# Optimization experiments

Measured on AMD Instinct MI355X. Metric: run time of the kernel, lower is better.

The kernel has to match this reference:

```python
import jax, jax.numpy as jnp
import numpy as np

B = 100000      # query points
L = 8           # num levels
N_RBF = 256     # RBF centers per level
F = 16          # features per level
OUT = 3         # output dim


def setup_inputs() -> dict:
    key = jax.random.key(0)
    k = jax.random.split(key, 6)
    x = jax.random.normal(k[0], (B, 3), dtype=jnp.float32)
    # small-magnitude features so gaussian RBF responses are non-degenerate
    feats = 0.1 * jax.random.normal(k[1], (B, L * F), dtype=jnp.float32)
    # centers initialized uniform(-1e-4, 1e-4) as in the torch module
    centers = jax.random.uniform(k[2], (L, N_RBF, F), dtype=jnp.float32,
                                 minval=-1e-4, maxval=1e-4)
    # log-width parameters (exp'd in forward); small perturbation around 0
    betas = 0.01 * jax.random.normal(k[3], (L, N_RBF, F), dtype=jnp.float32)
    W = jax.random.normal(k[4], (OUT, N_RBF * L), dtype=jnp.float32) / np.sqrt(N_RBF * L)
    b = jax.random.normal(k[5], (OUT,), dtype=jnp.float32) * 0.01
    return {"x": x, "feats": feats, "centers": centers, "betas": betas, "W": W, "b": b}


def reference(x, feats, centers, betas, W, b):
    # centers, betas: [L, N, F]. x is unused by the original forward (faithful).
    Lnum, N, f = centers.shape
    rbfs = []
    for i in range(Lnum):
        # concat of first i+1 per-level tables along feature axis -> [N, (i+1)*f]
        C = centers[: i + 1].transpose(1, 0, 2).reshape(N, (i + 1) * f)
        Bw = jnp.exp(betas[: i + 1].transpose(1, 0, 2).reshape(N, (i + 1) * f))
        x_in = feats[:, : (i + 1) * f]                      # [B, (i+1)*f]
        term1 = (x_in * x_in) @ Bw.T                        # [B, N]
        term2 = x_in @ (Bw * C).T                           # [B, N]
        term3 = jnp.sum(Bw * C * C, axis=1)                 # [N]
        dist_sq = term1 - 2.0 * term2 + term3[None, :]
        rbfs.append(jnp.exp(-0.5 * dist_sq))                # gaussian basis
    outs = jnp.concatenate(rbfs, axis=-1)                   # [B, L*N]
    return outs @ W.T + b
```

## Files before the change

### kernel.cpp

```cpp
#include <hip/hip_runtime.h>
#include <math.h>

#define LN 8
#define NRBF 256
#define FD 16
#define OUTD 3
#define KC (-0.72134752044f)

typedef __attribute__((ext_vector_type(8))) short short8;
typedef __attribute__((ext_vector_type(4))) float floatx4;
typedef __attribute__((ext_vector_type(2))) float floatx2;

__device__ __forceinline__ short f2bf(float f) {
    unsigned u = __builtin_bit_cast(unsigned, f);
    u += 0x7fffu + ((u >> 16) & 1u);
    return (short)(u >> 16);
}


__global__ __launch_bounds__(256) void prep(
    const float* __restrict__ centers, const float* __restrict__ betas,
    const float* __restrict__ W, short* __restrict__ PKB, float* __restrict__ EPI)
{
    __shared__ float ls[LN * 32];
    int blk = blockIdx.x;
    int tid = threadIdx.x;
    if (blk < 32) {
        int t = blk * 256 + tid;
        int lane = t & 63;
        int nt   = (t >> 6) & 15;
        int j    = t >> 10;
        int n    = nt * 16 + (lane & 15);
        int kq   = lane >> 4;
        size_t base = ((size_t)(j * NRBF + n)) * FD + kq * 4;
        float4 bq = *(const float4*)(betas + base);
        float4 cq = *(const float4*)(centers + base);
        float a0 = __expf(bq.x), a1 = __expf(bq.y), a2 = __expf(bq.z), a3 = __expf(bq.w);
        short8 v;
        v[0] = f2bf(a0); v[1] = f2bf(-2.0f * a0 * cq.x);
        v[2] = f2bf(a1); v[3] = f2bf(-2.0f * a1 * cq.y);
        v[4] = f2bf(a2); v[5] = f2bf(-2.0f * a2 * cq.z);
        v[6] = f2bf(a3); v[7] = f2bf(-2.0f * a3 * cq.w);
        *((short8*)(PKB + (size_t)((nt * 8 + j) * 64 + lane) * 8)) = v;
    } else {
        int jj = tid >> 5;
        int nl = tid & 31;
        int n  = (blk - 32) * 32 + nl;
        const float* bp = betas   + ((size_t)(jj * NRBF + n)) * FD;
        const float* cp = centers + ((size_t)(jj * NRBF + n)) * FD;
        float s = 0.f;
#pragma unroll
        for (int q = 0; q < 4; ++q) {
            float4 bq = *(const float4*)(bp + q * 4);
            float4 cq = *(const float4*)(cp + q * 4);
            s = fmaf(__expf(bq.x) * cq.x, cq.x, s);
            s = fmaf(__expf(bq.y) * cq.y, cq.y, s);
            s = fmaf(__expf(bq.z) * cq.z, cq.z, s);
            s = fmaf(__expf(bq.w) * cq.w, cq.w, s);
        }
        ls[jj * 32 + nl] = s;
        __syncthreads();
        float t3 = 0.f;
        for (int j2 = 0; j2 <= jj; ++j2) t3 += ls[j2 * 32 + nl];
        float4 e;
        e.x = KC * t3;
        e.y = W[0 * (LN * NRBF) + jj * NRBF + n];
        e.z = W[1 * (LN * NRBF) + jj * NRBF + n];
        e.w = W[2 * (LN * NRBF) + jj * NRBF + n];
        int nt = n >> 4, l = n & 15;
        ((float4*)EPI)[nt * 128 + jj * 16 + l] = e;
    }
}

__global__ __launch_bounds__(256, 4) void rbf_mfma(
    const float* __restrict__ feats, const short* __restrict__ PKB,
    const float* __restrict__ EPI, const float* __restrict__ bias,
    float* __restrict__ out, int B)
{
    int tid  = threadIdx.x;
    int lane = tid & 63;
    int wid  = tid >> 6;
    int ntile_total = (B + 15) >> 4;
    int tile = blockIdx.x * 4 + wid;
    bool tvalid = (tile < ntile_total);
    if (!tvalid) tile = ntile_total - 1;
    int b0 = tile * 16;
    int m  = lane & 15;
    int kq = lane >> 4;

    int brow = b0 + m; if (brow >= B) brow = B - 1;
    const float* xrow = feats + (size_t)brow * (LN * FD) + kq * 4;
    short8 afrag[LN];
#pragma unroll
    for (int j = 0; j < LN; ++j) {
        float4 x = *((const float4*)(xrow + j * FD));
        short8 f;
        f[0] = f2bf(x.x * x.x); f[1] = f2bf(x.x);
        f[2] = f2bf(x.y * x.y); f[3] = f2bf(x.y);
        f[4] = f2bf(x.z * x.z); f[5] = f2bf(x.z);
        f[6] = f2bf(x.w * x.w); f[7] = f2bf(x.w);
        afrag[j] = f;
    }

    floatx2 o01[4];
    float   o2[4];
#pragma unroll
    for (int r = 0; r < 4; ++r) { o01[r] = (floatx2){0.f, 0.f}; o2[r] = 0.f; }

#pragma unroll 1
    for (int nt = 0; nt < 8; ++nt) {
        const short8* pb0 = (const short8*)PKB + (size_t)(nt * 8) * 64 + lane;
        const short8* pb1 = pb0 + (size_t)8 * 8 * 64;
        const float4* ep0 = (const float4*)EPI + (size_t)nt * 128 + m;
        const float4* ep1 = ep0 + (size_t)8 * 128;
        floatx4 acc0 = {0.f, 0.f, 0.f, 0.f};
        floatx4 acc1 = {0.f, 0.f, 0.f, 0.f};
#pragma unroll
        for (int j = 0; j < LN; ++j) {
            short8 bf0 = pb0[j * 64];
            short8 bf1 = pb1[j * 64];
            float4 e0  = ep0[j * 16];
            float4 e1  = ep1[j * 16];
            acc0 = __builtin_amdgcn_mfma_f32_16x16x32_bf16(afrag[j], bf0, acc0, 0, 0, 0);
            acc1 = __builtin_amdgcn_mfma_f32_16x16x32_bf16(afrag[j], bf1, acc1, 0, 0, 0);
            floatx2 eyz0 = {e0.y, e0.z};
            floatx2 eyz1 = {e1.y, e1.z};
#pragma unroll
            for (int r = 0; r < 4; ++r) {
                float rv0 = __builtin_amdgcn_exp2f(fmaf(acc0[r], KC, e0.x));
                float rv1 = __builtin_amdgcn_exp2f(fmaf(acc1[r], KC, e1.x));
                floatx2 rv02 = {rv0, rv0};
                floatx2 rv12 = {rv1, rv1};
                o01[r] += rv02 * eyz0;
                o01[r] += rv12 * eyz1;
                o2[r]   = fmaf(rv0, e0.w, o2[r]);
                o2[r]   = fmaf(rv1, e1.w, o2[r]);
            }
        }
    }

    float oacc[12];
#pragma unroll
    for (int r = 0; r < 4; ++r) {
        oacc[r * 3 + 0] = o01[r].x;
        oacc[r * 3 + 1] = o01[r].y;
        oacc[r * 3 + 2] = o2[r];
    }
#pragma unroll
    for (int i = 0; i < 12; ++i) {
        oacc[i] += __shfl_xor(oacc[i], 1);
        oacc[i] += __shfl_xor(oacc[i], 2);
        oacc[i] += __shfl_xor(oacc[i], 4);
        oacc[i] += __shfl_xor(oacc[i], 8);
    }

    if (tvalid && m < OUTD) {
        float bv = bias[m];
#pragma unroll
        for (int r = 0; r < 4; ++r) {
            int row = b0 + kq * 4 + r;
            if (row < B) out[(size_t)row * OUTD + m] = oacc[r * 3 + m] + bv;
        }
    }
}

extern "C" void kernel_launch(void* const* d_in, const int* in_sizes, int n_in,
                              void* d_out, int out_size, void* d_ws, size_t ws_size,
                              hipStream_t stream) {
    const float* feats   = (const float*)d_in[1];
    const float* centers = (const float*)d_in[2];
    const float* betas   = (const float*)d_in[3];
    const float* W       = (const float*)d_in[4];
    const float* bias    = (const float*)d_in[5];
    float* out = (float*)d_out;
    int B = in_sizes[1] / (LN * FD);

    short* PKB = (short*)d_ws;
    float* EPI = (float*)((char*)d_ws + 65536 * 2);

    prep<<<40, 256, 0, stream>>>(centers, betas, W, PKB, EPI);

    int tiles  = (B + 15) / 16;
    int blocks = (tiles + 3) / 4;
    rbf_mfma<<<blocks, 256, 0, stream>>>(feats, PKB, EPI, bias, out, B);
}
```

Baseline: 161.1 us.

## Stage packed RBF weights in LDS via double-buffered async loads, loop levels outer

Reorders the main loop so the level index is outermost and all 16 N-tiles keep their accumulators live in registers. For each level, the packed B fragments and epilogue constants are staged into shared memory with double-buffered global_load_lds, so the four waves of a block share one copy instead of each wave loading from global/L2. The prep kernel's output layout is changed to match level-major staging. This adds 64 accumulator VGPRs and a barrier per level, and lowers the occupancy hint from 4 to 3 waves per SIMD.

```diff
diff --git a/kernel.cpp b/kernel.cpp
--- a/kernel.cpp
+++ b/kernel.cpp
@@ -41,7 +41,7 @@
         v[2] = f2bf(a1); v[3] = f2bf(-2.0f * a1 * cq.y);
         v[4] = f2bf(a2); v[5] = f2bf(-2.0f * a2 * cq.z);
         v[6] = f2bf(a3); v[7] = f2bf(-2.0f * a3 * cq.w);
-        *((short8*)(PKB + (size_t)((nt * 8 + j) * 64 + lane) * 8)) = v;
+        *((short8*)(PKB + (size_t)t * 8)) = v;
     } else {
         int jj = tid >> 5;
         int nl = tid & 31;
@@ -68,20 +68,23 @@
         e.z = W[1 * (LN * NRBF) + jj * NRBF + n];
         e.w = W[2 * (LN * NRBF) + jj * NRBF + n];
         int nt = n >> 4, l = n & 15;
-        ((float4*)EPI)[nt * 128 + jj * 16 + l] = e;
-    }
-}
-
-__global__ __launch_bounds__(256, 4) void rbf_mfma(
+        ((float4*)EPI)[(jj * 16 + nt) * 16 + l] = e;
+    }
+}
+
+__global__ __launch_bounds__(256, 3) void rbf_mfma(
     const float* __restrict__ feats, const short* __restrict__ PKB,
     const float* __restrict__ EPI, const float* __restrict__ bias,
     float* __restrict__ out, int B)
 {
+    __shared__ short8 pk_s[2][16 * 64];
+    __shared__ float4 ep_s[2][16 * 16];
+
     int tid  = threadIdx.x;
     int lane = tid & 63;
-    int wid  = tid >> 6;
+    int w    = tid >> 6;
     int ntile_total = (B + 15) >> 4;
-    int tile = blockIdx.x * 4 + wid;
+    int tile = blockIdx.x * 4 + w;
     bool tvalid = (tile < ntile_total);
     if (!tvalid) tile = ntile_total - 1;
     int b0 = tile * 16;
@@ -102,42 +105,60 @@
         afrag[j] = f;
     }
 
+#define STAGE(buf, jv)                                                          \
+    do {                                                                        \
+        _Pragma("unroll")                                                       \
+        for (int i = 0; i < 4; ++i) {                                           \
+            const short* gp = PKB + ((size_t)(jv) * 1024 + (w * 4 + i) * 64 + lane) * 8; \
+            __builtin_amdgcn_global_load_lds(                                   \
+                (const __attribute__((address_space(1))) void*)gp,              \
+                (__attribute__((address_space(3))) void*)&pk_s[buf][(w * 4 + i) * 64], \
+                16, 0, 0);                                                      \
+        }                                                                       \
+        const float* ge = EPI + ((size_t)(jv) * 256 + w * 64 + lane) * 4;       \
+        __builtin_amdgcn_global_load_lds(                                       \
+            (const __attribute__((address_space(1))) void*)ge,                  \
+            (__attribute__((address_space(3))) void*)&ep_s[buf][w * 64],        \
+            16, 0, 0);                                                          \
+    } while (0)
+
+    floatx4 acc[16];
+#pragma unroll
+    for (int nt = 0; nt < 16; ++nt) acc[nt] = (floatx4){0.f, 0.f, 0.f, 0.f};
+
     floatx2 o01[4];
     float   o2[4];
 #pragma unroll
     for (int r = 0; r < 4; ++r) { o01[r] = (floatx2){0.f, 0.f}; o2[r] = 0.f; }
 
-#pragma unroll 1
-    for (int nt = 0; nt < 8; ++nt) {
-        const short8* pb0 = (const short8*)PKB + (size_t)(nt * 8) * 64 + lane;
-        const short8* pb1 = pb0 + (size_t)8 * 8 * 64;
-        const float4* ep0 = (const float4*)EPI + (size_t)nt * 128 + m;
-        const float4* ep1 = ep0 + (size_t)8 * 128;
-        floatx4 acc0 = {0.f, 0.f, 0.f, 0.f};
-        floatx4 acc1 = {0.f, 0.f, 0.f, 0.f};
-#pragma unroll
-        for (int j = 0; j < LN; ++j) {
-            short8 bf0 = pb0[j * 64];
-            short8 bf1 = pb1[j * 64];
-            float4 e0  = ep0[j * 16];
-            float4 e1  = ep1[j * 16];
-            acc0 = __builtin_amdgcn_mfma_f32_16x16x32_bf16(afrag[j], bf0, acc0, 0, 0, 0);
-            acc1 = __builtin_amdgcn_mfma_f32_16x16x32_bf16(afrag[j], bf1, acc1, 0, 0, 0);
-            floatx2 eyz0 = {e0.y, e0.z};
-            floatx2 eyz1 = {e1.y, e1.z};
+    STAGE(0, 0);
+    __syncthreads();
+
+#pragma unroll
+    for (int j = 0; j < LN; ++j) {
+        int cur = j & 1;
+        if (j < LN - 1) STAGE(cur ^ 1, j + 1);
+
+#pragma unroll
+        for (int nt = 0; nt < 16; ++nt) {
+            short8 bf = pk_s[cur][nt * 64 + lane];
+            acc[nt] = __builtin_amdgcn_mfma_f32_16x16x32_bf16(afrag[j], bf, acc[nt], 0, 0, 0);
+        }
+
+#pragma unroll
+        for (int nt = 0; nt < 16; ++nt) {
+            float4 e = ep_s[cur][nt * 16 + m];
+            floatx2 eyz = {e.y, e.z};
 #pragma unroll
             for (int r = 0; r < 4; ++r) {
-                float rv0 = __builtin_amdgcn_exp2f(fmaf(acc0[r], KC, e0.x));
-                float rv1 = __builtin_amdgcn_exp2f(fmaf(acc1[r], KC, e1.x));
-                floatx2 rv02 = {rv0, rv0};
-                floatx2 rv12 = {rv1, rv1};
-                o01[r] += rv02 * eyz0;
-                o01[r] += rv12 * eyz1;
-                o2[r]   = fmaf(rv0, e0.w, o2[r]);
-                o2[r]   = fmaf(rv1, e1.w, o2[r]);
+                float rv = __builtin_amdgcn_exp2f(fmaf(acc[nt][r], KC, e.x));
+                o01[r] += (floatx2){rv, rv} * eyz;
+                o2[r]   = fmaf(rv, e.w, o2[r]);
             }
         }
-    }
+        __syncthreads();
+    }
+#undef STAGE
 
     float oacc[12];
 #pragma unroll
```

Result: faster. 142.6 us (-11.5%).
